# Optimization experiments

Hardware: AMD Instinct MI355X
Metric: run time of the kernel (lower is better)

Reference implementation:

```python
import jax, jax.numpy as jnp
import numpy as np

EPS = 1e-7
PI = np.pi


def _vel_to_R(vel):
    # vel: [..., 3] -> rotation matrix [..., 3, 3] (ZY convention from spherical angles)
    rho = jnp.linalg.norm(vel, axis=-1, keepdims=True)
    theta = jnp.arctan2(vel[..., 1:2], vel[..., 0:1])
    theta = theta + (theta < 0).astype(theta.dtype) * (2.0 * PI)  # symmetric_theta=False
    phi = jnp.arccos(jnp.clip(vel[..., 2:3] / (rho + EPS), -1.0, 1.0))
    ct, st = jnp.cos(theta)[..., 0], jnp.sin(theta)[..., 0]
    cp, sp = jnp.cos(phi)[..., 0], jnp.sin(phi)[..., 0]
    z = jnp.zeros_like(ct)
    R = jnp.stack([
        jnp.stack([cp * ct, -st, sp * ct], -1),
        jnp.stack([cp * st, ct, sp * st], -1),
        jnp.stack([-sp, z, cp], -1),
    ], -2)
    return R


def _rotate(R, x):
    return jnp.einsum('...ij,...j->...i', R, x)


def setup_inputs() -> dict:
    key = jax.random.key(0)
    B, N, H, D = 128, 100, 128, 3
    in_size = 2 * D  # 6
    nef = 3 * D + D * (D - 1) // 2 + in_size  # 18 edge features
    ks = jax.random.split(key, 12)

    inputs = jax.random.normal(ks[0], (B, N, in_size), jnp.float32)

    # fully connected edges (no self loops)
    send_np, recv_np = np.nonzero(~np.eye(N, dtype=bool))
    send_edges = jnp.asarray(send_np, jnp.int32)
    recv_edges = jnp.asarray(recv_np, jnp.int32)

    def lin(k, fin, fout):
        return jax.random.normal(k, (fin, fout), jnp.float32) / np.sqrt(fin)

    return dict(
        inputs=inputs,
        W1=lin(ks[1], nef, H), b1=jnp.zeros((H,), jnp.float32),
        W2=lin(ks[2], H, H), b2=jnp.zeros((H,), jnp.float32),
        Wr=lin(ks[3], in_size, H), br=jnp.zeros((H,), jnp.float32),
        W3=lin(ks[4], H, H), b3=jnp.zeros((H,), jnp.float32),
        W4=lin(ks[5], H, H), b4=jnp.zeros((H,), jnp.float32),
        W5=lin(ks[6], H, in_size), b5=jnp.zeros((in_size,), jnp.float32),
        send_edges=send_edges, recv_edges=recv_edges,
    )


def reference(inputs, W1, b1, W2, b2, Wr, br, W3, b3, W4, b4, W5, b5,
              send_edges, recv_edges):
    D = 3
    B, N, _ = inputs.shape

    # ---- Localizer.canonicalize_inputs ----
    vel = inputs[..., D:2 * D]
    Rnode = _vel_to_R(vel)                       # [B,N,3,3]
    Rinv_node = jnp.swapaxes(Rnode, -1, -2)
    canon_vel = _rotate(Rinv_node, vel)
    rel_feat = jnp.concatenate([jnp.zeros_like(canon_vel), canon_vel], -1)  # [B,N,6]

    # ---- Localizer.create_edge_attr ----
    x_j = inputs[:, send_edges]                  # [B,E,6] senders
    x_i = inputs[:, recv_edges]                  # [B,E,6] receivers
    R = _vel_to_R(x_i[..., D:2 * D])
    R_inv = jnp.swapaxes(R, -1, -2)
    rel_pos = x_j[..., :D] - x_i[..., :D]
    rot_rel = _rotate(R_inv, rel_pos)
    send_R = _vel_to_R(x_j[..., D:2 * D])
    rot_or = R_inv @ send_R
    euler = jnp.stack([
        jnp.arctan2(rot_or[..., 1, 0], rot_or[..., 0, 0]),
        jnp.arcsin(-rot_or[..., 2, 0]),
        jnp.arctan2(rot_or[..., 2, 1], rot_or[..., 2, 2]),
    ], -1) / PI
    dist = jnp.linalg.norm(rel_pos, axis=-1, keepdims=True)
    rho_e = jnp.linalg.norm(rot_rel, axis=-1, keepdims=True)
    theta_e = jnp.arctan2(rot_rel[..., 1:2], rot_rel[..., 0:1])  # symmetric theta
    phi_e = jnp.arccos(jnp.clip(rot_rel[..., 2:3] / (rho_e + EPS), -1.0, 1.0))
    rot_vel = _rotate(R_inv, x_j[..., D:2 * D])
    edge_attr = jnp.concatenate(
        [rot_rel, euler, dist, theta_e, phi_e, rot_vel], -1)   # [B,E,12]
    edge_attr = jnp.concatenate([edge_attr, rel_feat[:, recv_edges]], -1)  # [B,E,18]

    # ---- GNN: edge MLP + scatter-mean + out MLP (dropout off in eval) ----
    h = jax.nn.silu(edge_attr @ W1 + b1) @ W2 + b2               # [B,E,H]
    agg = jnp.zeros((B, N, h.shape[-1]), h.dtype).at[:, recv_edges].add(h)
    cnt = jnp.zeros((N,), h.dtype).at[recv_edges].add(1.0)
    agg = agg / jnp.maximum(cnt, 1.0)[None, :, None]             # scatter mean
    aug = agg + rel_feat @ Wr + br
    p = jax.nn.relu(aug @ W3 + b3)
    p = jax.nn.relu(p @ W4 + b4)
    pred = p @ W5 + b5                                           # [B,N,6]

    # ---- Globalizer: rotate each 3-vector chunk back to global frame ----
    gl = jnp.concatenate(
        [_rotate(Rnode, pred[..., i:i + D]) for i in range(0, pred.shape[-1], D)], -1)
    return inputs + gl
```

## Files before the change

### kernel.cpp

```cpp
#include <hip/hip_runtime.h>
#include <math.h>

#define EPSF 1e-7f
constexpr int NN  = 100;
constexpr int DEG = 99;
constexpr int IN  = 6;
constexpr int H   = 128;
constexpr int G   = 4;
constexpr float INV_PI = 0.3183098861837907f;
constexpr float LOG2E  = 1.4426950408889634f;
constexpr float LN2    = 0.6931471805599453f;

typedef __attribute__((ext_vector_type(4))) _Float16 half4;
typedef __attribute__((ext_vector_type(8))) _Float16 half8;
typedef __attribute__((ext_vector_type(4))) float f32x4;

constexpr int XST = 144;
constexpr int SXS = 15;
constexpr int TS  = 50;
constexpr int NT  = 25;

__device__ __forceinline__ float clampf(float x, float lo, float hi) {
    return fminf(fmaxf(x, lo), hi);
}
__device__ __forceinline__ float sig2(float y) {
    return __builtin_amdgcn_rcpf(1.f + __builtin_amdgcn_exp2f(-y));
}
__device__ __forceinline__ float fast_atan2(float y, float x) {
    float ax = fabsf(x), ay = fabsf(y);
    float mx = fmaxf(ax, ay), mn = fminf(ax, ay);
    float r = mn * __builtin_amdgcn_rcpf(fmaxf(mx, 1e-35f));
    float r2 = r * r;
    float p = fmaf(r2, -0.0851330f, 0.1801410f);
    p = fmaf(r2, p, -0.3302995f);
    p = fmaf(r2, p, 0.9998660f);
    float t = r * p;
    t = (ay > ax) ? (1.5707963267948966f - t) : t;
    t = (x < 0.f) ? (3.14159265358979323f - t) : t;
    return copysignf(t, y);
}
__device__ __forceinline__ float fast_asin(float z) {
    return fast_atan2(z, sqrtf(fmaxf(0.f, (1.f - z) * (1.f + z))));
}
__device__ __forceinline__ float fast_acos(float z) {
    return fast_atan2(sqrtf(fmaxf(0.f, (1.f - z) * (1.f + z))), z);
}
__device__ __forceinline__ void vel_to_R(float vx, float vy, float vz, float* R) {
    float rho = sqrtf(vx * vx + vy * vy + vz * vz);
    float rxy = sqrtf(vx * vx + vy * vy);
    float inv = __builtin_amdgcn_rcpf(rxy);
    bool big = rxy > 1e-30f;
    float ct = big ? vx * inv : 1.f;
    float st = big ? vy * inv : 0.f;
    float cp = clampf(vz * __builtin_amdgcn_rcpf(rho + EPSF), -1.f, 1.f);
    float sp = sqrtf(fmaxf(0.f, 1.f - cp * cp));
    R[0] = cp * ct; R[1] = -st; R[2] = sp * ct;
    R[3] = cp * st; R[4] = ct;  R[5] = sp * st;
    R[6] = -sp;     R[7] = 0.f; R[8] = cp;
}

__global__ void conv_w(const float* __restrict__ W1, const float* __restrict__ W2,
                       const float* __restrict__ W3, const float* __restrict__ W4,
                       half4* __restrict__ w1f, half8* __restrict__ wmlp) {
    int t = blockIdx.x * blockDim.x + threadIdx.x;
    if (t >= 104 * 64) return;
    int L = t & 63, f = t >> 6;
    int m = L & 15, qd = L >> 4;
    if (f < 8) {
        int n = f * 16 + m;
        half4 v;
#pragma unroll
        for (int j = 0; j < 4; ++j) {
            int k = qd * 4 + j;
            v[j] = (k < 12) ? (_Float16)(W1[k * H + n] * LOG2E) : (_Float16)0.f;
        }
        w1f[f * 64 + L] = v;
    } else {
        int ff = f - 8;
        int layer = ff >> 5, rest = ff & 31;
        int kt = rest >> 3, nt = rest & 7;
        const float* W = (layer == 0) ? W2 : (layer == 1) ? W3 : W4;
        float scale = (layer == 0) ? LN2 : 1.f;
        int n = nt * 16 + m;
        half8 v;
#pragma unroll
        for (int j = 0; j < 8; ++j)
            v[j] = (_Float16)(W[(kt * 32 + qd * 8 + j) * H + n] * scale);
        wmlp[((layer * 4 + kt) * 8 + nt) * 64 + L] = v;
    }
}

__global__ __launch_bounds__(128)
void locs_fused(const float* __restrict__ in,
                const float* __restrict__ W1, const float* __restrict__ b1,
                const float* __restrict__ b2,
                const float* __restrict__ Wr, const float* __restrict__ br,
                const float* __restrict__ b3, const float* __restrict__ b4,
                const float* __restrict__ W5, const float* __restrict__ b5,
                const half4* __restrict__ w1f, const half8* __restrict__ wmlp,
                float* __restrict__ out) {
    __shared__ _Float16 hpool[NT * TS * 4];
    __shared__ float sxr[NN * SXS];
    __shared__ float xFp[G * 132];
    __shared__ float cvF[16];
    __shared__ float pbF[G * 96];
    __shared__ float predF[G * 8];

    const int tid = threadIdx.x;
    const int L   = tid & 63;
    const int wv  = tid >> 6;
    const int q   = L >> 4;
    const int lm  = L & 15;
    const int bn0 = blockIdx.x * G;
    const int bB  = bn0 / NN;
    const int n0  = bn0 - bB * NN;

    {
        half4 z = {0, 0, 0, 0};
        for (int i = tid; i < NT * TS; i += 128) *(half4*)&hpool[i * 4] = z;
    }
    if (tid < NN) {
        const float* xi = in + (bB * NN + tid) * IN;
        float R[9];
        float px = xi[0], py = xi[1], pz = xi[2];
        float vx = xi[3], vy = xi[4], vz = xi[5];
        vel_to_R(vx, vy, vz, R);
        float* dst = sxr + tid * SXS;
#pragma unroll
        for (int k = 0; k < 9; ++k) dst[k] = R[k];
        dst[9] = px; dst[10] = py; dst[11] = pz;
        dst[12] = vx; dst[13] = vy; dst[14] = vz;
    }
    __syncthreads();
    if (tid < G) {
        const float* rg = sxr + (n0 + tid) * SXS;
        float vx = rg[12], vy = rg[13], vz = rg[14];
        cvF[tid * 4 + 0] = rg[0] * vx + rg[3] * vy + rg[6] * vz;
        cvF[tid * 4 + 1] = rg[1] * vx + rg[4] * vy + rg[7] * vz;
        cvF[tid * 4 + 2] = rg[2] * vx + rg[5] * vy + rg[8] * vz;
    }
    __syncthreads();

    float bs[4];
    {
        float cv0 = cvF[q * 4 + 0], cv1 = cvF[q * 4 + 1], cv2 = cvF[q * 4 + 2];
#pragma unroll
        for (int i = 0; i < 4; ++i) {
            int ch = wv * 64 + i * 16 + lm;
            bs[i] = (b1[ch] + cv0 * W1[15 * H + ch] + cv1 * W1[16 * H + ch]
                   + cv2 * W1[17 * H + ch]) * LOG2E;
        }
    }
    half4 bfr[4];
#pragma unroll
    for (int i = 0; i < 4; ++i) bfr[i] = w1f[(wv * 4 + i) * 64 + L];

#pragma unroll
    for (int rnd = 0; rnd < 4; ++rnd) {
        int j = tid + rnd * 128;
        if (j < G * DEG) {
            int g = j / DEG;
            int e = j - g * DEG;
            int nG = n0 + g;
            int s = e < nG ? e : e + 1;
            const float* rn = sxr + nG * SXS;
            const float* rs = sxr + s * SXS;
            float Rn[9];
#pragma unroll
            for (int k = 0; k < 9; ++k) Rn[k] = rn[k];
            float rel0 = rs[9] - rn[9], rel1 = rs[10] - rn[10], rel2 = rs[11] - rn[11];
            float vjx = rs[12], vjy = rs[13], vjz = rs[14];
            float Rs0 = rs[0], Rs1 = rs[1], Rs2 = rs[2];
            float Rs3 = rs[3], Rs4 = rs[4], Rs5 = rs[5];
            float Rs6 = rs[6], Rs7 = rs[7], Rs8 = rs[8];
            float rr0 = Rn[0] * rel0 + Rn[3] * rel1 + Rn[6] * rel2;
            float rr1 = Rn[1] * rel0 + Rn[4] * rel1 + Rn[7] * rel2;
            float rr2 = Rn[2] * rel0 + Rn[5] * rel1 + Rn[8] * rel2;
            float ro00 = Rn[0] * Rs0 + Rn[3] * Rs3 + Rn[6] * Rs6;
            float ro10 = Rn[1] * Rs0 + Rn[4] * Rs3 + Rn[7] * Rs6;
            float ro20 = Rn[2] * Rs0 + Rn[5] * Rs3 + Rn[8] * Rs6;
            float ro21 = Rn[2] * Rs1 + Rn[5] * Rs4 + Rn[8] * Rs7;
            float ro22 = Rn[2] * Rs2 + Rn[5] * Rs5 + Rn[8] * Rs8;
            float dist = sqrtf(rel0 * rel0 + rel1 * rel1 + rel2 * rel2);
            half4 f0, f1, f2;
            f0[0] = (_Float16)rr0; f0[1] = (_Float16)rr1; f0[2] = (_Float16)rr2;
            f0[3] = (_Float16)(fast_atan2(ro10, ro00) * INV_PI);
            f1[0] = (_Float16)(fast_asin(clampf(-ro20, -1.f, 1.f)) * INV_PI);
            f1[1] = (_Float16)(fast_atan2(ro21, ro22) * INV_PI);
            f1[2] = (_Float16)dist;
            f1[3] = (_Float16)fast_atan2(rr1, rr0);
            f2[0] = (_Float16)fast_acos(clampf(rr2 * __builtin_amdgcn_rcpf(dist + EPSF), -1.f, 1.f));
            f2[1] = (_Float16)(Rn[0] * vjx + Rn[3] * vjy + Rn[6] * vjz);
            f2[2] = (_Float16)(Rn[1] * vjx + Rn[4] * vjy + Rn[7] * vjz);
            f2[3] = (_Float16)(Rn[2] * vjx + Rn[5] * vjy + Rn[8] * vjz);
            int t = e >> 2;
            int mrow = g * 4 + (e & 3);
            _Float16* dst = hpool + (t * TS + mrow) * 4;
            *(half4*)(dst +   0)      = f0;
            *(half4*)(dst + 16 * 4)   = f1;
            *(half4*)(dst + 32 * 4)   = f2;
        }
    }
    __syncthreads();

    {
        float part[4] = {0.f, 0.f, 0.f, 0.f};
        f32x4 c[4];
#pragma unroll
        for (int i = 0; i < 4; ++i) c[i] = (f32x4){bs[i], bs[i], bs[i], bs[i]};
        const int loff = (q < 3) ? (q * 16 + lm) : 48;
        half4 a_cur = *(const half4*)&hpool[(0 * TS + loff) * 4];
#pragma unroll
        for (int t = 0; t < NT; ++t) {
            half4 a_next;
            if (t < NT - 1) a_next = *(const half4*)&hpool[((t + 1) * TS + loff) * 4];
            f32x4 d0 = __builtin_amdgcn_mfma_f32_16x16x16f16(a_cur, bfr[0], c[0], 0, 0, 0);
            f32x4 d1 = __builtin_amdgcn_mfma_f32_16x16x16f16(a_cur, bfr[1], c[1], 0, 0, 0);
            f32x4 d2 = __builtin_amdgcn_mfma_f32_16x16x16f16(a_cur, bfr[2], c[2], 0, 0, 0);
            f32x4 d3 = __builtin_amdgcn_mfma_f32_16x16x16f16(a_cur, bfr[3], c[3], 0, 0, 0);
#pragma unroll
            for (int r = 0; r < 4; ++r) {
                part[0] += d0[r] * sig2(d0[r]);
                part[1] += d1[r] * sig2(d1[r]);
                part[2] += d2[r] * sig2(d2[r]);
                part[3] += d3[r] * sig2(d3[r]);
            }
            a_cur = a_next;
        }
#pragma unroll
        for (int i = 0; i < 4; ++i)
            xFp[q * 132 + wv * 64 + i * 16 + lm] = part[i] - bs[i] * sig2(bs[i]);
    }
    __syncthreads();

    _Float16* xh = hpool;
#pragma unroll
    for (int layer = 0; layer < 3; ++layer) {
#pragma unroll
        for (int r = 0; r < G; ++r)
            xh[r * XST + tid] = (_Float16)xFp[r * 132 + tid];
        half8 bh[16];
#pragma unroll
        for (int kt = 0; kt < 4; ++kt) {
            int base = ((layer * 4 + kt) * 8 + wv * 4) * 64 + L;
#pragma unroll
            for (int i = 0; i < 4; ++i) bh[kt * 4 + i] = wmlp[base + i * 64];
        }
        __syncthreads();
        int rowb = (lm & 3) * XST;
        half8 ah[4];
#pragma unroll
        for (int kt = 0; kt < 4; ++kt)
            ah[kt] = *(const half8*)&xh[rowb + kt * 32 + q * 8];
        f32x4 acc[4];
#pragma unroll
        for (int i = 0; i < 4; ++i) acc[i] = (f32x4){0.f, 0.f, 0.f, 0.f};
#pragma unroll
        for (int kt = 0; kt < 4; ++kt)
#pragma unroll
            for (int i = 0; i < 4; ++i)
                acc[i] = __builtin_amdgcn_mfma_f32_16x16x32_f16(ah[kt], bh[kt * 4 + i],
                                                                acc[i], 0, 0, 0);
        __syncthreads();
        if (L < 16) {
#pragma unroll
            for (int i = 0; i < 4; ++i) {
                int ch = wv * 64 + i * 16 + lm;
                if (layer == 0) {
                    float b2c = b2[ch], brc = br[ch];
                    float w3c = Wr[3 * H + ch], w4c = Wr[4 * H + ch], w5c = Wr[5 * H + ch];
#pragma unroll
                    for (int r = 0; r < 4; ++r)
                        xFp[r * 132 + ch] = acc[i][r] * (1.f / 99.f) + b2c
                                          + cvF[r * 4 + 0] * w3c + cvF[r * 4 + 1] * w4c
                                          + cvF[r * 4 + 2] * w5c + brc;
                } else {
                    float bb = (layer == 1) ? b3[ch] : b4[ch];
#pragma unroll
                    for (int r = 0; r < 4; ++r)
                        xFp[r * 132 + ch] = fmaxf(0.f, acc[i][r] + bb);
                }
            }
        }
        __syncthreads();
    }

    if (tid < 96) {
        int o = tid >> 4, sl = tid & 15, kb = sl * 8;
        float w5[8];
#pragma unroll
        for (int j = 0; j < 8; ++j) w5[j] = W5[(kb + j) * IN + o];
#pragma unroll
        for (int g = 0; g < G; ++g) {
            float s = 0.f;
#pragma unroll
            for (int j = 0; j < 8; ++j) s = fmaf(xFp[g * 132 + kb + j], w5[j], s);
            pbF[g * 96 + sl * 6 + o] = s;
        }
    }
    __syncthreads();
    if (tid < 24) {
        int g = tid / 6, o = tid - g * 6;
        float s = b5[o];
#pragma unroll
        for (int sl = 0; sl < 16; ++sl) s += pbF[g * 96 + sl * 6 + o];
        predF[g * 8 + o] = s;
    }
    __syncthreads();
    if (tid < 24) {
        int g = tid / 6, o = tid - g * 6;
        int r = (o < 3) ? o : o - 3;
        int off = (o < 3) ? 0 : 3;
        const float* Rg = sxr + (n0 + g) * SXS;
        float gl = Rg[r * 3 + 0] * predF[g * 8 + off + 0]
                 + Rg[r * 3 + 1] * predF[g * 8 + off + 1]
                 + Rg[r * 3 + 2] * predF[g * 8 + off + 2];
        int bng = bn0 + g;
        out[bng * IN + o] = Rg[9 + o] + gl;
    }
}

extern "C" void kernel_launch(void* const* d_in, const int* in_sizes, int n_in,
                              void* d_out, int out_size, void* d_ws, size_t ws_size,
                              hipStream_t stream) {
    const float* in = (const float*)d_in[0];
    const float* W1 = (const float*)d_in[1];
    const float* b1 = (const float*)d_in[2];
    const float* W2 = (const float*)d_in[3];
    const float* b2 = (const float*)d_in[4];
    const float* Wr = (const float*)d_in[5];
    const float* br = (const float*)d_in[6];
    const float* W3 = (const float*)d_in[7];
    const float* b3 = (const float*)d_in[8];
    const float* W4 = (const float*)d_in[9];
    const float* b4 = (const float*)d_in[10];
    const float* W5 = (const float*)d_in[11];
    const float* b5 = (const float*)d_in[12];
    float* out = (float*)d_out;

    half4* w1f  = (half4*)d_ws;
    half8* wmlp = (half8*)((char*)d_ws + 4096);

    const int BN = in_sizes[0] / IN;
    conv_w<<<26, 256, 0, stream>>>(W1, W2, W3, W4, w1f, wmlp);
    locs_fused<<<BN / G, 128, 0, stream>>>(in, W1, b1, b2, Wr, br, b3, b4,
                                           W5, b5, w1f, wmlp, out);
}
```

Measured before the change: 142.8 us.

## Use 256-thread blocks splitting output channels across four waves

Doubles the block size to four wavefronts, and each wave now computes 32 output channels instead of 64 in the edge-MLP and node-MLP stages. Edge feature generation is spread over more threads in fewer rounds, and the node-frame velocity is computed directly by the thread that owns that node, which removes one barrier. The aim is more parallelism per block and less per-thread work and register use, at the cost of more threads competing for the same shared memory and barriers, and the remaining code must still be correct for 256 threads.

```diff
diff --git a/kernel.cpp b/kernel.cpp
--- a/kernel.cpp
+++ b/kernel.cpp
@@ -90,7 +90,7 @@
     }
 }
 
-__global__ __launch_bounds__(128)
+__global__ __launch_bounds__(256, 8)
 void locs_fused(const float* __restrict__ in,
                 const float* __restrict__ W1, const float* __restrict__ b1,
                 const float* __restrict__ b2,
@@ -117,7 +117,7 @@
 
     {
         half4 z = {0, 0, 0, 0};
-        for (int i = tid; i < NT * TS; i += 128) *(half4*)&hpool[i * 4] = z;
+        for (int i = tid; i < NT * TS; i += 256) *(half4*)&hpool[i * 4] = z;
     }
     if (tid < NN) {
         const float* xi = in + (bB * NN + tid) * IN;
@@ -130,34 +130,32 @@
         for (int k = 0; k < 9; ++k) dst[k] = R[k];
         dst[9] = px; dst[10] = py; dst[11] = pz;
         dst[12] = vx; dst[13] = vy; dst[14] = vz;
-    }
-    __syncthreads();
-    if (tid < G) {
-        const float* rg = sxr + (n0 + tid) * SXS;
-        float vx = rg[12], vy = rg[13], vz = rg[14];
-        cvF[tid * 4 + 0] = rg[0] * vx + rg[3] * vy + rg[6] * vz;
-        cvF[tid * 4 + 1] = rg[1] * vx + rg[4] * vy + rg[7] * vz;
-        cvF[tid * 4 + 2] = rg[2] * vx + rg[5] * vy + rg[8] * vz;
-    }
-    __syncthreads();
-
-    float bs[4];
+        int g = tid - n0;
+        if ((unsigned)g < (unsigned)G) {
+            cvF[g * 4 + 0] = R[0] * vx + R[3] * vy + R[6] * vz;
+            cvF[g * 4 + 1] = R[1] * vx + R[4] * vy + R[7] * vz;
+            cvF[g * 4 + 2] = R[2] * vx + R[5] * vy + R[8] * vz;
+        }
+    }
+    __syncthreads();
+
+    float bs[2];
     {
         float cv0 = cvF[q * 4 + 0], cv1 = cvF[q * 4 + 1], cv2 = cvF[q * 4 + 2];
 #pragma unroll
-        for (int i = 0; i < 4; ++i) {
-            int ch = wv * 64 + i * 16 + lm;
+        for (int i = 0; i < 2; ++i) {
+            int ch = wv * 32 + i * 16 + lm;
             bs[i] = (b1[ch] + cv0 * W1[15 * H + ch] + cv1 * W1[16 * H + ch]
                    + cv2 * W1[17 * H + ch]) * LOG2E;
         }
     }
-    half4 bfr[4];
-#pragma unroll
-    for (int i = 0; i < 4; ++i) bfr[i] = w1f[(wv * 4 + i) * 64 + L];
-
-#pragma unroll
-    for (int rnd = 0; rnd < 4; ++rnd) {
-        int j = tid + rnd * 128;
+    half4 bfr[2];
+#pragma unroll
+    for (int i = 0; i < 2; ++i) bfr[i] = w1f[(wv * 2 + i) * 64 + L];
+
+#pragma unroll
+    for (int rnd = 0; rnd < 2; ++rnd) {
+        int j = tid + rnd * 256;
         if (j < G * DEG) {
             int g = j / DEG;
             int e = j - g * DEG;
@@ -204,10 +202,10 @@
     __syncthreads();
 
     {
-        float part[4] = {0.f, 0.f, 0.f, 0.f};
-        f32x4 c[4];
-#pragma unroll
-        for (int i = 0; i < 4; ++i) c[i] = (f32x4){bs[i], bs[i], bs[i], bs[i]};
+        float part[2] = {0.f, 0.f};
+        f32x4 c[2];
+#pragma unroll
+        for (int i = 0; i < 2; ++i) c[i] = (f32x4){bs[i], bs[i], bs[i], bs[i]};
         const int loff = (q < 3) ? (q * 16 + lm) : 48;
         half4 a_cur = *(const half4*)&hpool[(0 * TS + loff) * 4];
 #pragma unroll
@@ -216,35 +214,36 @@
             if (t < NT - 1) a_next = *(const half4*)&hpool[((t + 1) * TS + loff) * 4];
             f32x4 d0 = __builtin_amdgcn_mfma_f32_16x16x16f16(a_cur, bfr[0], c[0], 0, 0, 0);
             f32x4 d1 = __builtin_amdgcn_mfma_f32_16x16x16f16(a_cur, bfr[1], c[1], 0, 0, 0);
-            f32x4 d2 = __builtin_amdgcn_mfma_f32_16x16x16f16(a_cur, bfr[2], c[2], 0, 0, 0);
-            f32x4 d3 = __builtin_amdgcn_mfma_f32_16x16x16f16(a_cur, bfr[3], c[3], 0, 0, 0);
 #pragma unroll
             for (int r = 0; r < 4; ++r) {
                 part[0] += d0[r] * sig2(d0[r]);
                 part[1] += d1[r] * sig2(d1[r]);
-                part[2] += d2[r] * sig2(d2[r]);
-                part[3] += d3[r] * sig2(d3[r]);
             }
             a_cur = a_next;
         }
 #pragma unroll
-        for (int i = 0; i < 4; ++i)
-            xFp[q * 132 + wv * 64 + i * 16 + lm] = part[i] - bs[i] * sig2(bs[i]);
+        for (int i = 0; i < 2; ++i)
+            xFp[q * 132 + wv * 32 + i * 16 + lm] = part[i] - bs[i] * sig2(bs[i]);
     }
     __syncthreads();
 
     _Float16* xh = hpool;
 #pragma unroll
     for (int layer = 0; layer < 3; ++layer) {
-#pragma unroll
-        for (int r = 0; r < G; ++r)
-            xh[r * XST + tid] = (_Float16)xFp[r * 132 + tid];
-        half8 bh[16];
+        {
+            int col = tid & 127, rh = tid >> 7;
+#pragma unroll
+            for (int r = 0; r < 2; ++r) {
+                int row = r * 2 + rh;
+                xh[row * XST + col] = (_Float16)xFp[row * 132 + col];
+            }
+        }
+        half8 bh[8];
 #pragma unroll
         for (int kt = 0; kt < 4; ++kt) {
-            int base = ((layer * 4 + kt) * 8 + wv * 4) * 64 + L;
-#pragma unroll
-            for (int i = 0; i < 4; ++i) bh[kt * 4 + i] = wmlp[base + i * 64];
+            int base = ((layer * 4 + kt) * 8 + wv * 2) * 64 + L;
+#pragma unroll
+            for (int i = 0; i < 2; ++i) bh[kt * 2 + i] = wmlp[base + i * 64];
         }
         __syncthreads();
         int rowb = (lm & 3) * XST;
@@ -252,20 +251,20 @@
 #pragma unroll
         for (int kt = 0; kt < 4; ++kt)
             ah[kt] = *(const half8*)&xh[rowb + kt * 32 + q * 8];
-        f32x4 acc[4];
-#pragma unroll
-        for (int i = 0; i < 4; ++i) acc[i] = (f32x4){0.f, 0.f, 0.f, 0.f};
+        f32x4 acc[2];
+#pragma unroll
+        for (int i = 0; i < 2; ++i) acc[i] = (f32x4){0.f, 0.f, 0.f, 0.f};
 #pragma unroll
         for (int kt = 0; kt < 4; ++kt)
 #pragma unroll
-            for (int i = 0; i < 4; ++i)
-                acc[i] = __builtin_amdgcn_mfma_f32_16x16x32_f16(ah[kt], bh[kt * 4 + i],
+            for (int i = 0; i < 2; ++i)
+                acc[i] = __builtin_amdgcn_mfma_f32_16x16x32_f16(ah[kt], bh[kt * 2 + i],
                                                                 acc[i], 0, 0, 0);
         __syncthreads();
         if (L < 16) {
 #pragma unroll
-            for (int i = 0; i < 4; ++i) {
-                int ch = wv * 64 + i * 16 + lm;
+            for (int i = 0; i < 2; ++i) {
+                int ch = (wv * 2 + i) * 16 + lm;
                 if (layer == 0) {
                     float b2c = b2[ch], brc = br[ch];
                     float w3c = Wr[3 * H + ch], w4c = Wr[4 * H + ch], w5c = Wr[5 * H + ch];
@@ -343,6 +342,6 @@
 
     const int BN = in_sizes[0] / IN;
     conv_w<<<26, 256, 0, stream>>>(W1, W2, W3, W4, w1f, wmlp);
-    locs_fused<<<BN / G, 128, 0, stream>>>(in, W1, b1, b2, Wr, br, b3, b4,
+    locs_fused<<<BN / G, 256, 0, stream>>>(in, W1, b1, b2, Wr, br, b3, b4,
                                            W5, b5, w1f, wmlp, out);
 }
```

Measured after the change: 127.3 us. 1.12x faster.
